# Performance work log

Measured on AMD Instinct MI355X. Metric: run time of the kernel, lower is better.

The kernel has to match this reference:

```python
import jax, jax.numpy as jnp
import numpy as np

B, S, D, H = 4, 2048, 1024, 16
DQ = D // H  # 64


def setup_inputs() -> dict:
    key = jax.random.key(0)
    ks = jax.random.split(key, 7)
    return {
        "q": jax.random.normal(ks[0], (B, S, D), dtype=jnp.float32),
        "k": jax.random.normal(ks[1], (B, S, D), dtype=jnp.float32),
        "v": jax.random.normal(ks[2], (B, S, D), dtype=jnp.float32),
        "mask": jax.random.randint(ks[3], (B, 1, S, S), 0, 2, dtype=jnp.int32),
        "weight_q": jax.random.normal(ks[4], (H, D, DQ), dtype=jnp.float32),
        "weight_k": jax.random.normal(ks[5], (H, D, DQ), dtype=jnp.float32),
        "weight_v": jax.random.normal(ks[6], (H, D, DQ), dtype=jnp.float32),
    }


def reference(q, k, v, mask, weight_q, weight_k, weight_v):
    # Per-head projections: [b,s,d] x [h,d,q] -> [b,h,s,q]
    Q = jnp.einsum('bsd,hdq->bhsq', q, weight_q)
    K = jnp.einsum('bsd,hdq->bhsq', k, weight_k)
    V = jnp.einsum('bsd,hdq->bhsq', v, weight_v)
    scale = 1.0 / jnp.sqrt(jnp.float32(DQ))
    scores = jnp.einsum('bhsq,bhtq->bhst', Q, K) * scale  # [b,h,s,s]
    scores = jnp.where(mask == 0, jnp.float32(-1e9), scores)
    scores = jax.nn.softmax(scores, axis=-1)
    # Faithful to torch.einsum('bhss,bhsq->bhsq', ...): repeated index 's'
    # takes the DIAGONAL of the attention matrix, scaling V elementwise.
    diag = jnp.diagonal(scores, axis1=2, axis2=3)  # [b,h,s]
    x = diag[..., None] * V  # [b,h,s,dq]
    return x
```

## Files before the change

### kernel.cpp

```cpp
#include <hip/hip_runtime.h>


#define BB 4
#define SS 2048
#define DD 1024
#define HH 16
#define DQQ 64

typedef unsigned short u16;
typedef unsigned int u32;
typedef __attribute__((ext_vector_type(8))) short bf16x8;
typedef __attribute__((ext_vector_type(4))) float f32x4;

static constexpr float SCALE_L2E = 0.125f * 1.44269504f;
static constexpr float NEG9 = -1e9f;

#define MFMA16(a, b, c) __builtin_amdgcn_mfma_f32_16x16x32_bf16((a), (b), (c), 0, 0, 0)

__device__ __forceinline__ float ex2(float x) {
#if __has_builtin(__builtin_amdgcn_exp2f)
    return __builtin_amdgcn_exp2f(x);
#else
    return __expf(x * 0.69314718055994531f);
#endif
}

__device__ __forceinline__ u16 bfrne(float x) {
    u32 u = __float_as_uint(x);
    return (u16)((u + 0x7fffu + ((u >> 16) & 1u)) >> 16);
}
__device__ __forceinline__ u32 pk2(float a, float b) {
    return (u32)bfrne(a) | ((u32)bfrne(b) << 16);
}
__device__ __forceinline__ float lo_f(u32 p) { return __uint_as_float(p << 16); }
__device__ __forceinline__ float hi_f(u32 p) { return __uint_as_float(p & 0xFFFF0000u); }

union U4V { u32 u[4]; bf16x8 v; uint4 q4; };

__global__ __launch_bounds__(256) void mask_pack_k(const int* __restrict__ mask,
                                                   u32* __restrict__ bits) {
    const int w = blockIdx.x * 256 + threadIdx.x;
    const long long row  = (long long)(w >> 6);
    const long long base = row * SS + (long long)((w & 63) << 5);
    const int4* mp = reinterpret_cast<const int4*>(mask + base);
    u32 v = 0;
#pragma unroll
    for (int j = 0; j < 8; ++j) {
        int4 m4 = mp[j];
        v |= (m4.x != 0 ? 1u : 0u) << (4 * j + 0);
        v |= (m4.y != 0 ? 1u : 0u) << (4 * j + 1);
        v |= (m4.z != 0 ? 1u : 0u) << (4 * j + 2);
        v |= (m4.w != 0 ? 1u : 0u) << (4 * j + 3);
    }
    bits[w] = v;
}

__global__ __launch_bounds__(256) void wsplit2_k(const float* __restrict__ W,
                                                 u16* __restrict__ Ph,
                                                 u16* __restrict__ Pl,
                                                 int has_lo, float scale) {
    const int f = blockIdx.x * 4 + (threadIdx.x >> 6);
    const int lane = threadIdx.x & 63;
    const int qtile = f >> 5, kc = f & 31;
    const int h = qtile >> 2, q = ((qtile & 3) << 4) + (lane & 15);
    const int d0 = kc * 32 + (lane >> 4) * 8;
    float x[8];
#pragma unroll
    for (int j = 0; j < 8; ++j)
        x[j] = W[((long long)h * DD + d0 + j) * DQQ + q] * scale;
    U4V hh;
    hh.u[0] = pk2(x[0], x[1]); hh.u[1] = pk2(x[2], x[3]);
    hh.u[2] = pk2(x[4], x[5]); hh.u[3] = pk2(x[6], x[7]);
    const long long base = ((long long)f << 9) + lane * 8;
    *reinterpret_cast<uint4*>(Ph + base) = hh.q4;
    if (has_lo) {
        U4V ll;
        ll.u[0] = pk2(x[0] - lo_f(hh.u[0]), x[1] - hi_f(hh.u[0]));
        ll.u[1] = pk2(x[2] - lo_f(hh.u[1]), x[3] - hi_f(hh.u[1]));
        ll.u[2] = pk2(x[4] - lo_f(hh.u[2]), x[5] - hi_f(hh.u[2]));
        ll.u[3] = pk2(x[6] - lo_f(hh.u[3]), x[7] - hi_f(hh.u[3]));
        *reinterpret_cast<uint4*>(Pl + base) = ll.q4;
    }
}

__global__ __launch_bounds__(256) void splitx_k(const float* __restrict__ X,
                                                u16* __restrict__ Xh,
                                                u16* __restrict__ Xl,
                                                int has_lo) {
    const int g = blockIdx.x * 256 + threadIdx.x;
    const int kc = g & 31;
    const int row = g >> 5;
    const float* xp = X + ((long long)row << 10) + kc * 32;
    const int lrow = row & 15;
    const long long base = (((long long)(row >> 4) * 32 + kc) << 9);
    float4 f[8];
#pragma unroll
    for (int i = 0; i < 8; ++i) f[i] = reinterpret_cast<const float4*>(xp)[i];
#pragma unroll
    for (int lg = 0; lg < 4; ++lg) {
        const float v0 = f[2 * lg].x, v1 = f[2 * lg].y, v2 = f[2 * lg].z, v3 = f[2 * lg].w;
        const float v4 = f[2 * lg + 1].x, v5 = f[2 * lg + 1].y,
                    v6 = f[2 * lg + 1].z, v7 = f[2 * lg + 1].w;
        U4V hh;
        hh.u[0] = pk2(v0, v1); hh.u[1] = pk2(v2, v3);
        hh.u[2] = pk2(v4, v5); hh.u[3] = pk2(v6, v7);
        const long long o = base + (lrow + 16 * lg) * 8;
        *reinterpret_cast<uint4*>(Xh + o) = hh.q4;
        if (has_lo) {
            U4V ll;
            ll.u[0] = pk2(v0 - lo_f(hh.u[0]), v1 - hi_f(hh.u[0]));
            ll.u[1] = pk2(v2 - lo_f(hh.u[1]), v3 - hi_f(hh.u[1]));
            ll.u[2] = pk2(v4 - lo_f(hh.u[2]), v5 - hi_f(hh.u[2]));
            ll.u[3] = pk2(v6 - lo_f(hh.u[3]), v7 - hi_f(hh.u[3]));
            *reinterpret_cast<uint4*>(Xl + o) = ll.q4;
        }
    }
}

__global__ __launch_bounds__(256) void proj_qk2_k(
        const u16* __restrict__ Xh, const u16* __restrict__ Xl,
        const u16* __restrict__ Wph, const u16* __restrict__ Wpl,
        u16* __restrict__ Oh, u16* __restrict__ Ol) {
    const int t = threadIdx.x, lane = t & 63, wid = t >> 6;
    const int lrow = lane & 15, lgrp = lane >> 4;
    const int qt0 = blockIdx.y * 8 + (wid >> 1) * 4;
    const int st0 = blockIdx.x * 8 + (wid & 1) * 4;

    f32x4 acc[4][4];
#pragma unroll
    for (int i = 0; i < 4; ++i)
#pragma unroll
        for (int j = 0; j < 4; ++j) acc[i][j] = (f32x4){0.f, 0.f, 0.f, 0.f};

#pragma unroll 2
    for (int kc = 0; kc < 32; ++kc) {
        bf16x8 Ah[4], Al[4], Bh[4], Bl[4];
#pragma unroll
        for (int mt = 0; mt < 4; ++mt) {
            const long long ab = (((long long)(qt0 + mt) * 32 + kc) << 9) + lane * 8;
            Ah[mt] = *reinterpret_cast<const bf16x8*>(Wph + ab);
            Al[mt] = *reinterpret_cast<const bf16x8*>(Wpl + ab);
        }
#pragma unroll
        for (int nt = 0; nt < 4; ++nt) {
            const long long bb = (((long long)(st0 + nt) * 32 + kc) << 9) + lane * 8;
            Bh[nt] = *reinterpret_cast<const bf16x8*>(Xh + bb);
            Bl[nt] = *reinterpret_cast<const bf16x8*>(Xl + bb);
        }
#pragma unroll
        for (int mt = 0; mt < 4; ++mt)
#pragma unroll
            for (int nt = 0; nt < 4; ++nt) {
                acc[mt][nt] = MFMA16(Ah[mt], Bh[nt], acc[mt][nt]);
                acc[mt][nt] = MFMA16(Ah[mt], Bl[nt], acc[mt][nt]);
                acc[mt][nt] = MFMA16(Al[mt], Bh[nt], acc[mt][nt]);
            }
    }

#pragma unroll
    for (int mt = 0; mt < 4; ++mt) {
        const int qtg = qt0 + mt;
        const int hh_ = qtg >> 2;
        const int qb = ((qtg & 3) << 4) + (lgrp << 2);
#pragma unroll
        for (int nt = 0; nt < 4; ++nt) {
            const int c = (st0 + nt) * 16 + lrow;
            const int b = c >> 11, s = c & 2047;
            const int bh = (b << 4) + hh_;
            const float x0 = acc[mt][nt][0], x1 = acc[mt][nt][1],
                        x2 = acc[mt][nt][2], x3 = acc[mt][nt][3];
            const u32 h01 = pk2(x0, x1), h23 = pk2(x2, x3);
            const u32 l01 = pk2(x0 - lo_f(h01), x1 - hi_f(h01));
            const u32 l23 = pk2(x2 - lo_f(h23), x3 - hi_f(h23));
            const int st = s >> 4, kcq = qb >> 5;
            const int lanep = lrow + (((qb & 31) >> 3) << 4);
            const long long oi = ((((long long)bh * 128 + st) * 2 + kcq) << 9)
                                 + lanep * 8 + (qb & 7);
            *reinterpret_cast<uint2*>(Oh + oi) = make_uint2(h01, h23);
            *reinterpret_cast<uint2*>(Ol + oi) = make_uint2(l01, l23);
        }
    }
}

__global__ __launch_bounds__(256) void proj_v2_k(
        const u16* __restrict__ Xh, const u16* __restrict__ Wph,
        u16* __restrict__ Vb) {
    const int t = threadIdx.x, lane = t & 63, wid = t >> 6;
    const int lrow = lane & 15, lgrp = lane >> 4;
    const int qt0 = blockIdx.y * 8 + (wid >> 1) * 4;
    const int st0 = blockIdx.x * 8 + (wid & 1) * 4;

    f32x4 acc[4][4];
#pragma unroll
    for (int i = 0; i < 4; ++i)
#pragma unroll
        for (int j = 0; j < 4; ++j) acc[i][j] = (f32x4){0.f, 0.f, 0.f, 0.f};

#pragma unroll 2
    for (int kc = 0; kc < 32; ++kc) {
        bf16x8 Ah[4], Bh[4];
#pragma unroll
        for (int mt = 0; mt < 4; ++mt) {
            const long long ab = (((long long)(qt0 + mt) * 32 + kc) << 9) + lane * 8;
            Ah[mt] = *reinterpret_cast<const bf16x8*>(Wph + ab);
        }
#pragma unroll
        for (int nt = 0; nt < 4; ++nt) {
            const long long bb = (((long long)(st0 + nt) * 32 + kc) << 9) + lane * 8;
            Bh[nt] = *reinterpret_cast<const bf16x8*>(Xh + bb);
        }
#pragma unroll
        for (int mt = 0; mt < 4; ++mt)
#pragma unroll
            for (int nt = 0; nt < 4; ++nt)
                acc[mt][nt] = MFMA16(Ah[mt], Bh[nt], acc[mt][nt]);
    }

#pragma unroll
    for (int mt = 0; mt < 4; ++mt) {
        const int qtg = qt0 + mt;
        const int hh_ = qtg >> 2;
        const int qb = ((qtg & 3) << 4) + (lgrp << 2);
#pragma unroll
        for (int nt = 0; nt < 4; ++nt) {
            const int c = (st0 + nt) * 16 + lrow;
            const int b = c >> 11, s = c & 2047;
            const int bh = (b << 4) + hh_;
            const u32 h01 = pk2(acc[mt][nt][0], acc[mt][nt][1]);
            const u32 h23 = pk2(acc[mt][nt][2], acc[mt][nt][3]);
            const long long oi = ((long long)bh * SS + s) * DQQ + qb;
            *reinterpret_cast<uint2*>(Vb + oi) = make_uint2(h01, h23);
        }
    }
}

__global__ __launch_bounds__(256) void attn_k(
        const u16* __restrict__ Qh, const u16* __restrict__ Ql,
        const u16* __restrict__ Kh, const u16* __restrict__ Kl,
        const u16* __restrict__ Vb, const u32* __restrict__ bits,
        float* __restrict__ out) {
    const int qt = blockIdx.x, h = blockIdx.y, b = blockIdx.z;
    const int s0 = qt * 64;
    const long long bh = b * HH + h;
    const int t = threadIdx.x, lane = t & 63, wid = t >> 6;
    const int l15 = lane & 15, lgrp = lane >> 4;

    __shared__ u16 Kst[2][4096];
    __shared__ float sdiag[64];
    __shared__ float dwgt[64];

    bf16x8 qfh[2], qfl[2];
#pragma unroll
    for (int ks = 0; ks < 2; ++ks) {
        const int stq = qt * 4 + wid;
        const long long gi = (((bh * 128 + stq) * 2 + ks) << 9) + lane * 8;
        qfh[ks] = *reinterpret_cast<const bf16x8*>(&Qh[gi]);
        qfl[ks] = *reinterpret_cast<const bf16x8*>(&Ql[gi]);
    }

    const u32 kbase = (u32)(bh * 131072u) + (u32)t * 8u;
    const u32 kfb   = (u32)(bh * 131072u) + (u32)lane * 8u;
    bf16x8 sh0, sh1;
    auto loadK = [&](int cchN) {
        const u32 o = kbase + (u32)cchN * 4096u;
        sh0 = *reinterpret_cast<const bf16x8*>(Kh + o);
        sh1 = *reinterpret_cast<const bf16x8*>(Kh + o + 2048u);
    };
    auto stageK = [&](int buf) {
        *reinterpret_cast<bf16x8*>(&Kst[buf][t * 8]) = sh0;
        *reinterpret_cast<bf16x8*>(&Kst[buf][(t + 256) * 8]) = sh1;
    };

    const u32* __restrict__ brow = bits + (((long long)b * SS + s0) << 6);
    u32 moff[4];
#pragma unroll
    for (int r = 0; r < 4; ++r)
        moff[r] = (u32)((wid * 16 + lgrp * 4 + r) << 6);

    const f32x4 zz = (f32x4){0.f, 0.f, 0.f, 0.f};

    {
        const int cA = qt, ntd = wid;
        const u32 o = kfb + (u32)cA * 4096u + (u32)(ntd * 2) * 512u;
        bf16x8 kh0 = *reinterpret_cast<const bf16x8*>(Kh + o);
        bf16x8 kh1 = *reinterpret_cast<const bf16x8*>(Kh + o + 512u);
        bf16x8 kl0 = *reinterpret_cast<const bf16x8*>(Kl + o);
        bf16x8 kl1 = *reinterpret_cast<const bf16x8*>(Kl + o + 512u);
        f32x4 a = MFMA16(qfh[0], kh0, zz);
        a = MFMA16(qfh[1], kh1, a);
        a = MFMA16(qfh[0], kl0, a);
        a = MFMA16(qfh[1], kl1, a);
        a = MFMA16(qfl[0], kh0, a);
        a = MFMA16(qfl[1], kh1, a);
#pragma unroll
        for (int r = 0; r < 4; ++r) {
            if (l15 == lgrp * 4 + r) {
                const u32 word = brow[moff[r] + (u32)(cA * 2) + (u32)(ntd >> 1)];
                const u32 bit = (word >> ((ntd & 1) * 16 + l15)) & 1u;
                sdiag[wid * 16 + lgrp * 4 + r] = bit ? a[r] : NEG9;
            }
        }
    }
    __syncthreads();

    float nsd[4];
    f32x4 msd;
    {
        float4 v4 = *reinterpret_cast<const float4*>(&sdiag[wid * 16 + lgrp * 4]);
        msd[0] = -v4.x; msd[1] = -v4.y; msd[2] = -v4.z; msd[3] = -v4.w;
        nsd[0] = NEG9 - v4.x; nsd[1] = NEG9 - v4.y;
        nsd[2] = NEG9 - v4.z; nsd[3] = NEG9 - v4.w;
    }

    loadK(0); stageK(0);
    float srun[4] = {0.f, 0.f, 0.f, 0.f};

    for (int cch = 0; cch < 32; ++cch) {
        const int cur = cch & 1;
        __syncthreads();
        if (cch + 1 < 32) loadK(cch + 1);

        uint2 mw[4];
        const u32 c2 = (u32)(cch * 2);
#pragma unroll
        for (int r = 0; r < 4; ++r)
            mw[r] = *reinterpret_cast<const uint2*>(brow + moff[r] + c2);

        const u32 ko = kfb + (u32)cch * 4096u;
#pragma unroll
        for (int nt = 0; nt < 4; ++nt) {
            bf16x8 kh0 = *reinterpret_cast<const bf16x8*>(&Kst[cur][(nt * 2 + 0) * 512 + lane * 8]);
            bf16x8 kh1 = *reinterpret_cast<const bf16x8*>(&Kst[cur][(nt * 2 + 1) * 512 + lane * 8]);
            bf16x8 kl0 = *reinterpret_cast<const bf16x8*>(Kl + ko + (u32)(nt * 2 + 0) * 512u);
            bf16x8 kl1 = *reinterpret_cast<const bf16x8*>(Kl + ko + (u32)(nt * 2 + 1) * 512u);
            f32x4 a = MFMA16(qfh[0], kh0, msd);
            a = MFMA16(qfh[1], kh1, a);
            a = MFMA16(qfh[0], kl0, a);
            a = MFMA16(qfh[1], kl1, a);
            a = MFMA16(qfl[0], kh0, a);
            a = MFMA16(qfl[1], kh1, a);
#pragma unroll
            for (int r = 0; r < 4; ++r) {
                const u32 w = (nt < 2) ? mw[r].x : mw[r].y;
                const float d = ((w >> ((nt & 1) * 16 + l15)) & 1u) ? a[r] : nsd[r];
                srun[r] += ex2(d);
            }
        }

        if (cch + 1 < 32) stageK(cur ^ 1);
    }

#pragma unroll
    for (int r = 0; r < 4; ++r) {
        float so = srun[r];
#pragma unroll
        for (int st = 1; st < 16; st <<= 1)
            so += __shfl_xor(so, st, 64);
        if (l15 == 0)
            dwgt[wid * 16 + lgrp * 4 + r] = 1.0f / so;
    }
    __syncthreads();

    const int orow = t >> 2, oc = (t & 3) * 16;
    const float w = dwgt[orow];
    const u16* vp = Vb + (bh * SS + s0 + orow) * DQQ + oc;
    float* op = out + (bh * SS + s0 + orow) * DQQ + oc;
#pragma unroll
    for (int j = 0; j < 4; ++j) {
        u32 pv = *reinterpret_cast<const u32*>(&vp[j * 4 + 0]);
        u32 pv2 = *reinterpret_cast<const u32*>(&vp[j * 4 + 2]);
        float4 o;
        o.x = lo_f(pv) * w;  o.y = hi_f(pv) * w;
        o.z = lo_f(pv2) * w; o.w = hi_f(pv2) * w;
        reinterpret_cast<float4*>(op)[j] = o;
    }
}

extern "C" void kernel_launch(void* const* d_in, const int* in_sizes, int n_in,
                              void* d_out, int out_size, void* d_ws, size_t ws_size,
                              hipStream_t stream) {
    (void)in_sizes; (void)n_in; (void)out_size; (void)ws_size;
    const float* q    = (const float*)d_in[0];
    const float* k    = (const float*)d_in[1];
    const float* v    = (const float*)d_in[2];
    const int*   mask = (const int*)d_in[3];
    const float* wq   = (const float*)d_in[4];
    const float* wk   = (const float*)d_in[5];
    const float* wv   = (const float*)d_in[6];

    const size_t NP2 = (size_t)BB * HH * SS * DQQ * 2;
    char* wsp = (char*)d_ws;
    u16* Qh = (u16*)wsp;            wsp += NP2;
    u16* Ql = (u16*)wsp;            wsp += NP2;
    u16* Kh = (u16*)wsp;            wsp += NP2;
    u16* Kl = (u16*)wsp;            wsp += NP2;
    u16* Vb = (u16*)wsp;            wsp += NP2;
    u16* Wph = (u16*)wsp;           wsp += (size_t)3 * 2048 * 512 * 2;
    u16* Wpl = (u16*)wsp;           wsp += (size_t)2 * 2048 * 512 * 2;
    u32* bits = (u32*)wsp;          wsp += (size_t)BB * SS * 64 * 4;
    u16* extra = (u16*)wsp;

    u16* Xh_q = Kh;    u16* Xl_q = Kl;
    u16* Xh_k = Vb;    u16* Xl_k = extra;
    u16* Xh_v = extra;

    mask_pack_k<<<dim3(2048), dim3(256), 0, stream>>>(mask, bits);
    wsplit2_k<<<dim3(512), dim3(256), 0, stream>>>(wq, Wph, Wpl, 1, SCALE_L2E);
    wsplit2_k<<<dim3(512), dim3(256), 0, stream>>>(wk, Wph + (1 << 20), Wpl + (1 << 20), 1, 1.0f);
    wsplit2_k<<<dim3(512), dim3(256), 0, stream>>>(wv, Wph + (2u << 20), Wph, 0, 1.0f);

    splitx_k<<<dim3(1024), dim3(256), 0, stream>>>(q, Xh_q, Xl_q, 1);
    proj_qk2_k<<<dim3(64, 8), dim3(256), 0, stream>>>(Xh_q, Xl_q, Wph, Wpl, Qh, Ql);

    splitx_k<<<dim3(1024), dim3(256), 0, stream>>>(k, Xh_k, Xl_k, 1);
    proj_qk2_k<<<dim3(64, 8), dim3(256), 0, stream>>>(Xh_k, Xl_k,
                                                      Wph + (1 << 20), Wpl + (1 << 20),
                                                      Kh, Kl);

    splitx_k<<<dim3(1024), dim3(256), 0, stream>>>(v, Xh_v, Xh_v, 0);
    proj_v2_k<<<dim3(64, 8), dim3(256), 0, stream>>>(Xh_v, Wph + (2u << 20), Vb);

    attn_k<<<dim3(32, 16, 4), dim3(256), 0, stream>>>(Qh, Ql, Kh, Kl, Vb, bits,
                                                      (float*)d_out);
}
```

Baseline: 343.5 us.

## Stage projection operand tiles through shared memory with register prefetch

The QK projection GEMM kernel now loads each k-chunk's weight and input fragments cooperatively into a 32KB LDS buffer, with every tile fetched once per block instead of by each of the two waves that need it. The next chunk is prefetched into registers while MFMAs run on the current one. This halves redundant global/L2 loads but adds two block barriers per iteration, more register pressure, and LDS usage that can reduce occupancy.

```diff
diff --git a/kernel.cpp b/kernel.cpp
--- a/kernel.cpp
+++ b/kernel.cpp
@@ -123,8 +123,38 @@
         u16* __restrict__ Oh, u16* __restrict__ Ol) {
     const int t = threadIdx.x, lane = t & 63, wid = t >> 6;
     const int lrow = lane & 15, lgrp = lane >> 4;
-    const int qt0 = blockIdx.y * 8 + (wid >> 1) * 4;
-    const int st0 = blockIdx.x * 8 + (wid & 1) * 4;
+    const int qtB = blockIdx.y * 8, stB = blockIdx.x * 8;
+    const int qt0 = qtB + (wid >> 1) * 4;
+    const int st0 = stB + (wid & 1) * 4;
+
+    __shared__ u16 Lf[32 * 512];
+
+    const u16* srcs[8];
+    u32 ldso[8];
+#pragma unroll
+    for (int j = 0; j < 8; ++j) {
+        const int tile = wid + 4 * j;
+        const u16* base;
+        int idx;
+        if (tile < 8)       { base = Wph; idx = qtB + tile; }
+        else if (tile < 16) { base = Wpl; idx = qtB + tile - 8; }
+        else if (tile < 24) { base = Xh;  idx = stB + tile - 16; }
+        else                { base = Xl;  idx = stB + tile - 24; }
+        srcs[j] = base + (((long long)idx * 32) << 9) + lane * 8;
+        ldso[j] = (u32)(tile * 512 + lane * 8);
+    }
+
+    uint4 rg[8];
+    auto loadS = [&](int kc) {
+#pragma unroll
+        for (int j = 0; j < 8; ++j)
+            rg[j] = *reinterpret_cast<const uint4*>(srcs[j] + kc * 512);
+    };
+    auto stageS = [&]() {
+#pragma unroll
+        for (int j = 0; j < 8; ++j)
+            *reinterpret_cast<uint4*>(&Lf[ldso[j]]) = rg[j];
+    };
 
     f32x4 acc[4][4];
 #pragma unroll
@@ -132,20 +162,22 @@
 #pragma unroll
         for (int j = 0; j < 4; ++j) acc[i][j] = (f32x4){0.f, 0.f, 0.f, 0.f};
 
-#pragma unroll 2
+    const int aT = (wid >> 1) * 4;
+    const int bT = 16 + (wid & 1) * 4;
+
+    loadS(0);
     for (int kc = 0; kc < 32; ++kc) {
+        stageS();
+        __syncthreads();
+        if (kc + 1 < 32) loadS(kc + 1);
+
         bf16x8 Ah[4], Al[4], Bh[4], Bl[4];
 #pragma unroll
-        for (int mt = 0; mt < 4; ++mt) {
-            const long long ab = (((long long)(qt0 + mt) * 32 + kc) << 9) + lane * 8;
-            Ah[mt] = *reinterpret_cast<const bf16x8*>(Wph + ab);
-            Al[mt] = *reinterpret_cast<const bf16x8*>(Wpl + ab);
-        }
-#pragma unroll
-        for (int nt = 0; nt < 4; ++nt) {
-            const long long bb = (((long long)(st0 + nt) * 32 + kc) << 9) + lane * 8;
-            Bh[nt] = *reinterpret_cast<const bf16x8*>(Xh + bb);
-            Bl[nt] = *reinterpret_cast<const bf16x8*>(Xl + bb);
+        for (int i = 0; i < 4; ++i) {
+            Ah[i] = *reinterpret_cast<const bf16x8*>(&Lf[(aT + i) * 512 + lane * 8]);
+            Al[i] = *reinterpret_cast<const bf16x8*>(&Lf[(aT + i + 8) * 512 + lane * 8]);
+            Bh[i] = *reinterpret_cast<const bf16x8*>(&Lf[(bT + i) * 512 + lane * 8]);
+            Bl[i] = *reinterpret_cast<const bf16x8*>(&Lf[(bT + i + 8) * 512 + lane * 8]);
         }
 #pragma unroll
         for (int mt = 0; mt < 4; ++mt)
@@ -155,6 +187,7 @@
                 acc[mt][nt] = MFMA16(Ah[mt], Bl[nt], acc[mt][nt]);
                 acc[mt][nt] = MFMA16(Al[mt], Bh[nt], acc[mt][nt]);
             }
+        __syncthreads();
     }
 
 #pragma unroll
```

Result: slower. 534.1 us (+55.5%).
